# Optimization experiments

Hardware: AMD Instinct MI355X
Metric: run time of the kernel (lower is better)

Reference implementation:

```python
import jax, jax.numpy as jnp
import numpy as np

B, HQ, HKV, QL, SL = 2, 32, 8, 1024, 4096
HEAD_DIM, HALF, ROPE, RANK = 128, 64, 64, 512


def setup_inputs() -> dict:
    key = jax.random.key(0)
    ks = jax.random.split(key, 6)
    return {
        "Q": jax.random.normal(ks[0], (B, HQ, QL, HEAD_DIM), jnp.float32),
        "C_kv_t2": jax.random.normal(ks[1], (B, SL, RANK), jnp.float32),
        "K_rope_t2": jax.random.normal(ks[2], (B, HKV, SL, ROPE), jnp.float32),
        "U_l": jax.random.normal(ks[3], (HALF, HALF), jnp.float32) / 8.0,
        "W_UK": jax.random.normal(ks[4], (HEAD_DIM - ROPE, RANK), jnp.float32) / 8.0,
        "W_UV": jax.random.normal(ks[5], (RANK, HEAD_DIM), jnp.float32) / 8.0,
    }


def reference(Q, C_kv_t2, K_rope_t2, U_l, W_UK, W_UV):
    # --- absorb_and_score ---
    # Rotate each half of Q by U_l (applied as x @ U_l.T)
    Qx, Qy = Q[..., :HALF], Q[..., HALF:]
    Q_rot = jnp.concatenate([Qx @ U_l.T, Qy @ U_l.T], axis=-1)  # [B,HQ,QL,HEAD_DIM]
    Q_rope = Q_rot[..., :ROPE]                                   # [B,HQ,QL,ROPE]
    Q_nope = Q_rot[..., ROPE:]                                   # [B,HQ,QL,nope_dim]
    Q_abs = Q_nope @ W_UK                                        # [B,HQ,QL,RANK]
    scores_nope = jnp.einsum('bhqr,bsr->bhqs', Q_abs, C_kv_t2)   # [B,HQ,QL,SL]
    # GQA: group q-heads per kv-head instead of materializing repeat_interleave
    g = HQ // HKV
    Qr_g = Q_rope.reshape(B, HKV, g, QL, ROPE)
    scores_rope = jnp.einsum('bkgqr,bksr->bkgqs', Qr_g, K_rope_t2)
    scores = scores_nope + scores_rope.reshape(B, HQ, QL, SL)
    # --- softmax glue + decompress_value ---
    weights = jax.nn.softmax(scores, axis=-1)                    # [B,HQ,QL,SL]
    out_latent = jnp.einsum('bhqs,bsr->bhqr', weights, C_kv_t2)  # [B,HQ,QL,RANK]
    out = out_latent @ W_UV                                      # [B,HQ,QL,HEAD_DIM]
    return out
```

## Files before the change

### kernel.cpp

```cpp
#include <hip/hip_runtime.h>
#include <stdint.h>

#define B_N   2
#define HQ_N  32
#define HKV_N 8
#define QL_N  1024
#define SL_N  4096
#define DH_N  128
#define ROPE_N 64
#define RANK_N 512

typedef _Float16 f16;
typedef _Float16 half8 __attribute__((ext_vector_type(8)));
typedef __fp16 fp16x2 __attribute__((ext_vector_type(2)));
typedef float floatx16 __attribute__((ext_vector_type(16)));
typedef int int2v __attribute__((ext_vector_type(2)));

union H8 { half8 h; uint64_t q[2]; };
union PK2 { fp16x2 h; uint32_t u; };
union BFU { uint32_t u[4]; half8 h; };

__device__ inline half8 cvt8(float4 a, float4 b) {
  half8 o;
  o[0] = (f16)a.x; o[1] = (f16)a.y; o[2] = (f16)a.z; o[3] = (f16)a.w;
  o[4] = (f16)b.x; o[5] = (f16)b.y; o[6] = (f16)b.z; o[7] = (f16)b.w;
  return o;
}

__global__ __launch_bounds__(256) void k_convert(const float* __restrict__ Kr,
                                                 f16* __restrict__ Krf) {
  size_t idx = ((size_t)blockIdx.x * 256 + threadIdx.x) * 8;
  float4 a = *(const float4*)(Kr + idx);
  float4 b = *(const float4*)(Kr + idx + 4);
  *(half8*)(Krf + idx) = cvt8(a, b);
}

__global__ __launch_bounds__(256) void k_weights(const float* __restrict__ Ul,
                                                 const float* __restrict__ WUK,
                                                 const float* __restrict__ WUV,
                                                 f16* __restrict__ M2T2,
                                                 f16* __restrict__ WUKh,
                                                 f16* __restrict__ WUVT) {
  int idx = blockIdx.x * 256 + threadIdx.x;
  if (idx < 16384) {
    int c = idx >> 7, d = idx & 127;
    float v = 0.f;
    if (c < 64) { if (d >= 64) v = Ul[c * 64 + (d - 64)]; }
    else        { if (d < 64)  v = Ul[(c - 64) * 64 + d]; }
    M2T2[idx] = (f16)v;
  } else if (idx < 49152) {
    int i = idx - 16384;
    WUKh[i] = (f16)WUK[i];
  } else {
    int i = idx - 49152;
    int c = i >> 9, r = i & 511;
    WUVT[i] = (f16)WUV[r * 128 + c];
  }
}

__global__ __launch_bounds__(256) void k_kncw(const float* __restrict__ C,
                                              const f16* __restrict__ WUKh,
                                              const f16* __restrict__ WUVT,
                                              f16* __restrict__ Kn,
                                              f16* __restrict__ CWT) {
  int t = threadIdx.x;
  int wave = t >> 6, lane = t & 63, l31 = lane & 31, lhi = lane >> 5;
  int b = blockIdx.x >> 7, st = blockIdx.x & 127;
  int s0 = st * 32;
  const float* cp = C + ((size_t)b * SL_N + s0 + l31) * RANK_N + lhi * 8;
  floatx16 a0, a1;
#pragma unroll
  for (int r = 0; r < 16; r++) { a0[r] = 0.f; a1[r] = 0.f; }
#pragma unroll 4
  for (int kk = 0; kk < 32; ++kk) {
    float4 fa = *(const float4*)(cp + kk * 16);
    float4 fb = *(const float4*)(cp + kk * 16 + 4);
    half8 cf = cvt8(fa, fb);
    if (wave == 0) {
      half8 b0 = *(const half8*)(WUKh + (size_t)l31 * RANK_N + kk * 16 + lhi * 8);
      half8 b1 = *(const half8*)(WUKh + (size_t)(32 + l31) * RANK_N + kk * 16 + lhi * 8);
      a0 = __builtin_amdgcn_mfma_f32_32x32x16_f16(cf, b0, a0, 0, 0, 0);
      a1 = __builtin_amdgcn_mfma_f32_32x32x16_f16(cf, b1, a1, 0, 0, 0);
    } else if (wave == 1) {
      half8 w0 = *(const half8*)(WUVT + (size_t)l31 * RANK_N + kk * 16 + lhi * 8);
      a0 = __builtin_amdgcn_mfma_f32_32x32x16_f16(w0, cf, a0, 0, 0, 0);
    } else if (wave == 2) {
      half8 w1 = *(const half8*)(WUVT + (size_t)(32 + l31) * RANK_N + kk * 16 + lhi * 8);
      half8 w2 = *(const half8*)(WUVT + (size_t)(64 + l31) * RANK_N + kk * 16 + lhi * 8);
      a0 = __builtin_amdgcn_mfma_f32_32x32x16_f16(w1, cf, a0, 0, 0, 0);
      a1 = __builtin_amdgcn_mfma_f32_32x32x16_f16(w2, cf, a1, 0, 0, 0);
    } else {
      half8 w3 = *(const half8*)(WUVT + (size_t)(96 + l31) * RANK_N + kk * 16 + lhi * 8);
      a0 = __builtin_amdgcn_mfma_f32_32x32x16_f16(w3, cf, a0, 0, 0, 0);
    }
  }
  if (wave == 0) {
#pragma unroll
    for (int r = 0; r < 16; r++) {
      int row = (r & 3) + 8 * (r >> 2) + 4 * lhi;
      Kn[((size_t)b * SL_N + s0 + row) * 64 + l31]      = (f16)a0[r];
      Kn[((size_t)b * SL_N + s0 + row) * 64 + 32 + l31] = (f16)a1[r];
    }
  } else if (wave == 1) {
#pragma unroll
    for (int r = 0; r < 16; r++) {
      int row = (r & 3) + 8 * (r >> 2) + 4 * lhi;
      CWT[((size_t)b * DH_N + row) * SL_N + s0 + l31] = (f16)a0[r];
    }
  } else if (wave == 2) {
#pragma unroll
    for (int r = 0; r < 16; r++) {
      int row = (r & 3) + 8 * (r >> 2) + 4 * lhi;
      CWT[((size_t)b * DH_N + 32 + row) * SL_N + s0 + l31] = (f16)a0[r];
      CWT[((size_t)b * DH_N + 64 + row) * SL_N + s0 + l31] = (f16)a1[r];
    }
  } else {
#pragma unroll
    for (int r = 0; r < 16; r++) {
      int row = (r & 3) + 8 * (r >> 2) + 4 * lhi;
      CWT[((size_t)b * DH_N + 96 + row) * SL_N + s0 + l31] = (f16)a0[r];
    }
  }
}

#define KROW 132
#define CROW 68

__global__ __launch_bounds__(256, 2) void k_flash(
    const float* __restrict__ Q, const f16* __restrict__ M2T2,
    const f16* __restrict__ Kn, const f16* __restrict__ Krf,
    const f16* __restrict__ CWT, float* __restrict__ out) {
  __shared__ __align__(16) char smem[51712];
  f16* kbuf  = (f16*)smem;
  f16* cbuf0 = (f16*)(smem + 16896);
  f16* cbuf1 = (f16*)(smem + 34304);
  f16* qs    = (f16*)smem;
  float* ot  = (float*)smem;

  int t = threadIdx.x;
  int wave = t >> 6, lane = t & 63, l31 = lane & 31, lhi = lane >> 5;
  int qt = blockIdx.x & 7; int h = (blockIdx.x >> 3) & 31; int b = blockIdx.x >> 8;
  int kv = h >> 2;
  int qloc = wave * 32 + l31;

  const f16* Knb = Kn + (size_t)b * SL_N * 64;
  const f16* Kb  = Krf + (size_t)(b * HKV_N + kv) * SL_N * ROPE_N;
  const f16* Wb  = CWT + (size_t)b * DH_N * SL_N;

  int kr = t >> 3, kc = t & 7;
  int cA = t >> 2, cch = t & 3;
  const f16* pKn = Knb + (size_t)kr * 64 + kc * 8;
  const f16* pKr = Kb + (size_t)kr * ROPE_N + kc * 8;
  const f16* pW0 = Wb + (size_t)cA * SL_N;
  const f16* pW1 = Wb + (size_t)(64 + cA) * SL_N;
  int sw0 = ((cch) ^ (cA & 7)) * 8;
  int sw1 = ((cch + 4) ^ (cA & 7)) * 8;
  int rsw = l31 & 7;

  H8 a0, a1, r0, r1, c0, c1, c2, c3;
  a0.h = *(const half8*)(pKn);
  a1.h = *(const half8*)(pKn + 32 * 64);
  r0.h = *(const half8*)(pKr);
  r1.h = *(const half8*)(pKr + 32 * ROPE_N);
  c0.h = *(const half8*)(pW0 + cch * 8);
  c1.h = *(const half8*)(pW0 + (cch + 4) * 8);
  c2.h = *(const half8*)(pW1 + cch * 8);
  c3.h = *(const half8*)(pW1 + (cch + 4) * 8);

  {
    const float* qp = Q + ((size_t)(b * HQ_N + h) * QL_N + qt * 128 + wave * 32 + l31) * DH_N + lhi * 8;
    floatx16 acc[4];
#pragma unroll
    for (int ct = 0; ct < 4; ct++)
#pragma unroll
      for (int r = 0; r < 16; r++) acc[ct][r] = 0.f;
#pragma unroll
    for (int kk = 0; kk < 8; ++kk) {
      float4 fa = *(const float4*)(qp + kk * 16);
      float4 fb = *(const float4*)(qp + kk * 16 + 4);
      half8 af = cvt8(fa, fb);
#pragma unroll
      for (int ct = 0; ct < 4; ct++) {
        half8 bf = *(const half8*)(M2T2 + (size_t)(ct * 32 + l31) * 128 + kk * 16 + lhi * 8);
        acc[ct] = __builtin_amdgcn_mfma_f32_32x32x16_f16(af, bf, acc[ct], 0, 0, 0);
      }
    }
    const float LOG2E = 1.44269504f;
#pragma unroll
    for (int ct = 0; ct < 4; ct++)
#pragma unroll
      for (int r = 0; r < 16; r++) {
        int row = (r & 3) + 8 * (r >> 2) + 4 * lhi;
        qs[(wave * 32 + row) * 132 + ct * 32 + l31] = (f16)(acc[ct][r] * LOG2E);
      }
  }
  __syncthreads();
  half8 qf[8];
#pragma unroll
  for (int kk = 0; kk < 8; kk++)
    qf[kk] = *(const half8*)(qs + (size_t)qloc * 132 + kk * 16 + lhi * 8);
  __syncthreads();

  {
    uint64_t* d;
    d = (uint64_t*)(kbuf + kr * KROW + kc * 8);              d[0] = a0.q[0]; d[1] = a0.q[1];
    d = (uint64_t*)(kbuf + (kr + 32) * KROW + kc * 8);       d[0] = a1.q[0]; d[1] = a1.q[1];
    d = (uint64_t*)(kbuf + kr * KROW + 64 + kc * 8);         d[0] = r0.q[0]; d[1] = r0.q[1];
    d = (uint64_t*)(kbuf + (kr + 32) * KROW + 64 + kc * 8);  d[0] = r1.q[0]; d[1] = r1.q[1];
    d = (uint64_t*)(cbuf0 + cA * CROW + sw0);                d[0] = c0.q[0]; d[1] = c0.q[1];
    d = (uint64_t*)(cbuf0 + cA * CROW + sw1);                d[0] = c1.q[0]; d[1] = c1.q[1];
    d = (uint64_t*)(cbuf0 + (64 + cA) * CROW + sw0);         d[0] = c2.q[0]; d[1] = c2.q[1];
    d = (uint64_t*)(cbuf0 + (64 + cA) * CROW + sw1);         d[0] = c3.q[0]; d[1] = c3.q[1];
  }
  __syncthreads();

  floatx16 oacc[4];
#pragma unroll
  for (int ct = 0; ct < 4; ct++)
#pragma unroll
    for (int r = 0; r < 16; r++) oacc[ct][r] = 0.f;
  float m_run = -1e30f, l_run = 0.f;

  for (int it = 0; it < 64; ++it) {
    f16* cc = (it & 1) ? cbuf1 : cbuf0;
    f16* cn = (it & 1) ? cbuf0 : cbuf1;
    bool pre = it < 63;
    int s0n = (it + 1) * 64;
    if (pre) {
      size_t ko = (size_t)s0n * 64;
      a0.h = *(const half8*)(pKn + ko);
      a1.h = *(const half8*)(pKn + ko + 32 * 64);
      r0.h = *(const half8*)(pKr + ko);
      r1.h = *(const half8*)(pKr + ko + 32 * ROPE_N);
      c0.h = *(const half8*)(pW0 + s0n + cch * 8);
      c1.h = *(const half8*)(pW0 + s0n + (cch + 4) * 8);
      c2.h = *(const half8*)(pW1 + s0n + cch * 8);
      c3.h = *(const half8*)(pW1 + s0n + (cch + 4) * 8);
    }

    floatx16 sa0, sa1;
#pragma unroll
    for (int r = 0; r < 16; r++) { sa0[r] = 0.f; sa1[r] = 0.f; }
    const f16* ka0 = kbuf + l31 * KROW + lhi * 8;
    const f16* ka1 = kbuf + (32 + l31) * KROW + lhi * 8;
    __builtin_amdgcn_s_setprio(1);
#pragma unroll
    for (int kk = 0; kk < 8; kk++) {
      H8 x0, x1;
      const uint64_t* p0 = (const uint64_t*)(ka0 + kk * 16);
      const uint64_t* p1 = (const uint64_t*)(ka1 + kk * 16);
      x0.q[0] = p0[0]; x0.q[1] = p0[1];
      x1.q[0] = p1[0]; x1.q[1] = p1[1];
      sa0 = __builtin_amdgcn_mfma_f32_32x32x16_f16(x0.h, qf[kk], sa0, 0, 0, 0);
      sa1 = __builtin_amdgcn_mfma_f32_32x32x16_f16(x1.h, qf[kk], sa1, 0, 0, 0);
    }
    __builtin_amdgcn_s_setprio(0);
    __syncthreads();

    float mt = -1e30f;
#pragma unroll
    for (int r = 0; r < 16; r++) { mt = fmaxf(mt, sa0[r]); mt = fmaxf(mt, sa1[r]); }
    mt = fmaxf(mt, __shfl_xor(mt, 32, 64));
    if (__any(mt > m_run)) {
      float m_new = fmaxf(m_run, mt);
      float alpha = __builtin_amdgcn_exp2f(m_run - m_new);
      l_run *= alpha;
#pragma unroll
      for (int ct = 0; ct < 4; ct++)
#pragma unroll
        for (int r = 0; r < 16; r++) oacc[ct][r] *= alpha;
      m_run = m_new;
    }
    float psum = 0.f;
#pragma unroll
    for (int r = 0; r < 16; r++) { sa0[r] = __builtin_amdgcn_exp2f(sa0[r] - m_run); psum += sa0[r]; }
#pragma unroll
    for (int r = 0; r < 16; r++) { sa1[r] = __builtin_amdgcn_exp2f(sa1[r] - m_run); psum += sa1[r]; }
    psum += __shfl_xor(psum, 32, 64);
    l_run += psum;

    half8 bfr0, bfr1, bfr2, bfr3;
    {
      uint32_t pk[8];
#pragma unroll
      for (int g = 0; g < 8; ++g) {
        PK2 pu; pu.h = __builtin_amdgcn_cvt_pkrtz(sa0[2 * g], sa0[2 * g + 1]);
        pk[g] = pu.u;
      }
      int2v v0 = __builtin_amdgcn_permlane32_swap((int)pk[0], (int)pk[2], false, false);
      pk[0] = (uint32_t)v0.x; pk[2] = (uint32_t)v0.y;
      int2v v1 = __builtin_amdgcn_permlane32_swap((int)pk[1], (int)pk[3], false, false);
      pk[1] = (uint32_t)v1.x; pk[3] = (uint32_t)v1.y;
      int2v v2 = __builtin_amdgcn_permlane32_swap((int)pk[4], (int)pk[6], false, false);
      pk[4] = (uint32_t)v2.x; pk[6] = (uint32_t)v2.y;
      int2v v3 = __builtin_amdgcn_permlane32_swap((int)pk[5], (int)pk[7], false, false);
      pk[5] = (uint32_t)v3.x; pk[7] = (uint32_t)v3.y;
      BFU f0, f1;
      f0.u[0] = pk[0]; f0.u[1] = pk[1]; f0.u[2] = pk[2]; f0.u[3] = pk[3];
      f1.u[0] = pk[4]; f1.u[1] = pk[5]; f1.u[2] = pk[6]; f1.u[3] = pk[7];
      bfr0 = f0.h; bfr1 = f1.h;
    }
    {
      uint32_t pk[8];
#pragma unroll
      for (int g = 0; g < 8; ++g) {
        PK2 pu; pu.h = __builtin_amdgcn_cvt_pkrtz(sa1[2 * g], sa1[2 * g + 1]);
        pk[g] = pu.u;
      }
      int2v v0 = __builtin_amdgcn_permlane32_swap((int)pk[0], (int)pk[2], false, false);
      pk[0] = (uint32_t)v0.x; pk[2] = (uint32_t)v0.y;
      int2v v1 = __builtin_amdgcn_permlane32_swap((int)pk[1], (int)pk[3], false, false);
      pk[1] = (uint32_t)v1.x; pk[3] = (uint32_t)v1.y;
      int2v v2 = __builtin_amdgcn_permlane32_swap((int)pk[4], (int)pk[6], false, false);
      pk[4] = (uint32_t)v2.x; pk[6] = (uint32_t)v2.y;
      int2v v3 = __builtin_amdgcn_permlane32_swap((int)pk[5], (int)pk[7], false, false);
      pk[5] = (uint32_t)v3.x; pk[7] = (uint32_t)v3.y;
      BFU f0, f1;
      f0.u[0] = pk[0]; f0.u[1] = pk[1]; f0.u[2] = pk[2]; f0.u[3] = pk[3];
      f1.u[0] = pk[4]; f1.u[1] = pk[5]; f1.u[2] = pk[6]; f1.u[3] = pk[7];
      bfr2 = f0.h; bfr3 = f1.h;
    }

    __builtin_amdgcn_s_setprio(1);
#pragma unroll
    for (int ks = 0; ks < 4; ++ks) {
      half8 bfh = (ks == 0) ? bfr0 : (ks == 1) ? bfr1 : (ks == 2) ? bfr2 : bfr3;
#pragma unroll
      for (int ct = 0; ct < 4; ct++) {
        H8 af;
        const uint64_t* pa = (const uint64_t*)(cc + (ct * 32 + l31) * CROW +
                                               (((ks * 2 + lhi) ^ rsw) * 8));
        af.q[0] = pa[0]; af.q[1] = pa[1];
        oacc[ct] = __builtin_amdgcn_mfma_f32_32x32x16_f16(af.h, bfh, oacc[ct], 0, 0, 0);
      }
    }
    __builtin_amdgcn_s_setprio(0);

    if (pre) {
      uint64_t* d;
      d = (uint64_t*)(kbuf + kr * KROW + kc * 8);              d[0] = a0.q[0]; d[1] = a0.q[1];
      d = (uint64_t*)(kbuf + (kr + 32) * KROW + kc * 8);       d[0] = a1.q[0]; d[1] = a1.q[1];
      d = (uint64_t*)(kbuf + kr * KROW + 64 + kc * 8);         d[0] = r0.q[0]; d[1] = r0.q[1];
      d = (uint64_t*)(kbuf + (kr + 32) * KROW + 64 + kc * 8);  d[0] = r1.q[0]; d[1] = r1.q[1];
      d = (uint64_t*)(cn + cA * CROW + sw0);                   d[0] = c0.q[0]; d[1] = c0.q[1];
      d = (uint64_t*)(cn + cA * CROW + sw1);                   d[0] = c1.q[0]; d[1] = c1.q[1];
      d = (uint64_t*)(cn + (64 + cA) * CROW + sw0);            d[0] = c2.q[0]; d[1] = c2.q[1];
      d = (uint64_t*)(cn + (64 + cA) * CROW + sw1);            d[0] = c3.q[0]; d[1] = c3.q[1];
    }
    __syncthreads();
  }

  float inv = 1.0f / l_run;
  float* outp = out + ((size_t)(b * HQ_N + h) * QL_N + qt * 128) * DH_N;
#pragma unroll
  for (int p = 0; p < 2; ++p) {
    __syncthreads();
    if ((qloc >> 6) == p) {
      int lr = qloc & 63;
#pragma unroll
      for (int ct = 0; ct < 4; ct++)
#pragma unroll
        for (int r = 0; r < 16; r++) {
          int c = ct * 32 + (r & 3) + 8 * (r >> 2) + 4 * lhi;
          ot[lr * 133 + c] = oacc[ct][r] * inv;
        }
    }
    __syncthreads();
#pragma unroll
    for (int i = 0; i < 8; i++) {
      int flat = i * 256 + t; int q = flat >> 5, ch = flat & 31;
      float4 v;
      v.x = ot[q * 133 + ch * 4 + 0];
      v.y = ot[q * 133 + ch * 4 + 1];
      v.z = ot[q * 133 + ch * 4 + 2];
      v.w = ot[q * 133 + ch * 4 + 3];
      *(float4*)(outp + (size_t)(p * 64 + q) * DH_N + ch * 4) = v;
    }
  }
}

extern "C" void kernel_launch(void* const* d_in, const int* in_sizes, int n_in,
                              void* d_out, int out_size, void* d_ws, size_t ws_size,
                              hipStream_t stream) {
  (void)in_sizes; (void)n_in; (void)out_size; (void)ws_size;
  const float* Q   = (const float*)d_in[0];
  const float* C   = (const float*)d_in[1];
  const float* Kr  = (const float*)d_in[2];
  const float* Ul  = (const float*)d_in[3];
  const float* WUK = (const float*)d_in[4];
  const float* WUV = (const float*)d_in[5];
  float* out = (float*)d_out;
  char* ws = (char*)d_ws;
  f16* Krf   = (f16*)ws;
  f16* CWT   = (f16*)(ws + 8388608);
  f16* Kn    = (f16*)(ws + 10485760);
  f16* M2T2  = (f16*)(ws + 11534336);
  f16* WUKh  = (f16*)(ws + 11567104);
  f16* WUVT  = (f16*)(ws + 11632640);

  hipLaunchKernelGGL(k_convert, dim3(2048), dim3(256), 0, stream, Kr, Krf);
  hipLaunchKernelGGL(k_weights, dim3(448),  dim3(256), 0, stream, Ul, WUK, WUV, M2T2, WUKh, WUVT);
  hipLaunchKernelGGL(k_kncw,    dim3(256),  dim3(256), 0, stream, C, WUKh, WUVT, Kn, CWT);
  hipLaunchKernelGGL(k_flash,   dim3(512),  dim3(256), 0, stream, Q, M2T2, Kn, Krf, CWT, out);
}
```

Before: 287.7 us.

## Software-pipeline score MMA with softmax and PV in flash kernel

Restructures the flash loop so the QK^T MFMA for tile t+1 is issued while softmax and the PV MFMA run for tile t. The K tile is now double-buffered in LDS and global loads are prefetched two tiles ahead. This is meant to hide softmax latency and global-load latency behind matrix work, at the cost of more LDS (68.6 KB per block) and more register pressure. The C_kv fp32-to-fp16 conversion moves into the convert kernel, which adds a separate pass over C, and the max/sum reductions are split into independent chains for more ILP.

```diff
diff --git a/kernel.cpp b/kernel.cpp
--- a/kernel.cpp
+++ b/kernel.cpp
@@ -27,12 +27,19 @@
   return o;
 }
 
-__global__ __launch_bounds__(256) void k_convert(const float* __restrict__ Kr,
+__global__ __launch_bounds__(256) void k_convert(const float* __restrict__ C,
+                                                 const float* __restrict__ Kr,
+                                                 f16* __restrict__ Cf,
                                                  f16* __restrict__ Krf) {
+  const size_t NC = (size_t)B_N * SL_N * RANK_N;
   size_t idx = ((size_t)blockIdx.x * 256 + threadIdx.x) * 8;
-  float4 a = *(const float4*)(Kr + idx);
-  float4 b = *(const float4*)(Kr + idx + 4);
-  *(half8*)(Krf + idx) = cvt8(a, b);
+  const float* src;
+  f16* dst;
+  if (idx < NC) { src = C + idx;         dst = Cf + idx; }
+  else          { src = Kr + (idx - NC); dst = Krf + (idx - NC); }
+  float4 a = *(const float4*)(src);
+  float4 b = *(const float4*)(src + 4);
+  *(half8*)dst = cvt8(a, b);
 }
 
 __global__ __launch_bounds__(256) void k_weights(const float* __restrict__ Ul,
@@ -58,7 +65,7 @@
   }
 }
 
-__global__ __launch_bounds__(256) void k_kncw(const float* __restrict__ C,
+__global__ __launch_bounds__(256) void k_kncw(const f16* __restrict__ Cf,
                                               const f16* __restrict__ WUKh,
                                               const f16* __restrict__ WUVT,
                                               f16* __restrict__ Kn,
@@ -67,15 +74,13 @@
   int wave = t >> 6, lane = t & 63, l31 = lane & 31, lhi = lane >> 5;
   int b = blockIdx.x >> 7, st = blockIdx.x & 127;
   int s0 = st * 32;
-  const float* cp = C + ((size_t)b * SL_N + s0 + l31) * RANK_N + lhi * 8;
+  const f16* cp = Cf + ((size_t)b * SL_N + s0 + l31) * RANK_N + lhi * 8;
   floatx16 a0, a1;
 #pragma unroll
   for (int r = 0; r < 16; r++) { a0[r] = 0.f; a1[r] = 0.f; }
 #pragma unroll 4
   for (int kk = 0; kk < 32; ++kk) {
-    float4 fa = *(const float4*)(cp + kk * 16);
-    float4 fb = *(const float4*)(cp + kk * 16 + 4);
-    half8 cf = cvt8(fa, fb);
+    half8 cf = *(const half8*)(cp + kk * 16);
     if (wave == 0) {
       half8 b0 = *(const half8*)(WUKh + (size_t)l31 * RANK_N + kk * 16 + lhi * 8);
       half8 b1 = *(const half8*)(WUKh + (size_t)(32 + l31) * RANK_N + kk * 16 + lhi * 8);
@@ -130,10 +135,11 @@
     const float* __restrict__ Q, const f16* __restrict__ M2T2,
     const f16* __restrict__ Kn, const f16* __restrict__ Krf,
     const f16* __restrict__ CWT, float* __restrict__ out) {
-  __shared__ __align__(16) char smem[51712];
-  f16* kbuf  = (f16*)smem;
-  f16* cbuf0 = (f16*)(smem + 16896);
-  f16* cbuf1 = (f16*)(smem + 34304);
+  __shared__ __align__(16) char smem[68608];
+  f16* kbuf0 = (f16*)smem;
+  f16* kbuf1 = (f16*)(smem + 16896);
+  f16* cbuf0 = (f16*)(smem + 33792);
+  f16* cbuf1 = (f16*)(smem + 51200);
   f16* qs    = (f16*)smem;
   float* ot  = (float*)smem;
 
@@ -157,18 +163,36 @@
   int sw1 = ((cch + 4) ^ (cA & 7)) * 8;
   int rsw = l31 & 7;
 
-  H8 a0, a1, r0, r1, c0, c1, c2, c3;
-  a0.h = *(const half8*)(pKn);
-  a1.h = *(const half8*)(pKn + 32 * 64);
-  r0.h = *(const half8*)(pKr);
-  r1.h = *(const half8*)(pKr + 32 * ROPE_N);
-  c0.h = *(const half8*)(pW0 + cch * 8);
-  c1.h = *(const half8*)(pW0 + (cch + 4) * 8);
-  c2.h = *(const half8*)(pW1 + cch * 8);
-  c3.h = *(const half8*)(pW1 + (cch + 4) * 8);
-
+  H8 a0, a1, r0, r1, c0v, c1v, c2v, c3v;
+
+  auto issue = [&](int t2) {
+    size_t ko = (size_t)t2 * (64 * 64);
+    int soff = t2 * 64;
+    a0.h  = *(const half8*)(pKn + ko);
+    a1.h  = *(const half8*)(pKn + ko + 32 * 64);
+    r0.h  = *(const half8*)(pKr + ko);
+    r1.h  = *(const half8*)(pKr + ko + 32 * 64);
+    c0v.h = *(const half8*)(pW0 + soff + cch * 8);
+    c1v.h = *(const half8*)(pW0 + soff + (cch + 4) * 8);
+    c2v.h = *(const half8*)(pW1 + soff + cch * 8);
+    c3v.h = *(const half8*)(pW1 + soff + (cch + 4) * 8);
+  };
+  auto commit = [&](f16* kbW, f16* cbW) {
+    uint64_t* d;
+    d = (uint64_t*)(kbW + kr * KROW + kc * 8);             d[0] = a0.q[0]; d[1] = a0.q[1];
+    d = (uint64_t*)(kbW + (kr + 32) * KROW + kc * 8);      d[0] = a1.q[0]; d[1] = a1.q[1];
+    d = (uint64_t*)(kbW + kr * KROW + 64 + kc * 8);        d[0] = r0.q[0]; d[1] = r0.q[1];
+    d = (uint64_t*)(kbW + (kr + 32) * KROW + 64 + kc * 8); d[0] = r1.q[0]; d[1] = r1.q[1];
+    d = (uint64_t*)(cbW + cA * CROW + sw0);                d[0] = c0v.q[0]; d[1] = c0v.q[1];
+    d = (uint64_t*)(cbW + cA * CROW + sw1);                d[0] = c1v.q[0]; d[1] = c1v.q[1];
+    d = (uint64_t*)(cbW + (64 + cA) * CROW + sw0);         d[0] = c2v.q[0]; d[1] = c2v.q[1];
+    d = (uint64_t*)(cbW + (64 + cA) * CROW + sw1);         d[0] = c3v.q[0]; d[1] = c3v.q[1];
+  };
+
+  issue(0);
+  half8 qf[8];
   {
-    const float* qp = Q + ((size_t)(b * HQ_N + h) * QL_N + qt * 128 + wave * 32 + l31) * DH_N + lhi * 8;
+    const float* qp = Q + ((size_t)(b * HQ_N + h) * QL_N + qt * 128 + qloc) * DH_N + lhi * 8;
     floatx16 acc[4];
 #pragma unroll
     for (int ct = 0; ct < 4; ct++)
@@ -195,25 +219,11 @@
       }
   }
   __syncthreads();
-  half8 qf[8];
 #pragma unroll
   for (int kk = 0; kk < 8; kk++)
     qf[kk] = *(const half8*)(qs + (size_t)qloc * 132 + kk * 16 + lhi * 8);
   __syncthreads();
 
-  {
-    uint64_t* d;
-    d = (uint64_t*)(kbuf + kr * KROW + kc * 8);              d[0] = a0.q[0]; d[1] = a0.q[1];
-    d = (uint64_t*)(kbuf + (kr + 32) * KROW + kc * 8);       d[0] = a1.q[0]; d[1] = a1.q[1];
-    d = (uint64_t*)(kbuf + kr * KROW + 64 + kc * 8);         d[0] = r0.q[0]; d[1] = r0.q[1];
-    d = (uint64_t*)(kbuf + (kr + 32) * KROW + 64 + kc * 8);  d[0] = r1.q[0]; d[1] = r1.q[1];
-    d = (uint64_t*)(cbuf0 + cA * CROW + sw0);                d[0] = c0.q[0]; d[1] = c0.q[1];
-    d = (uint64_t*)(cbuf0 + cA * CROW + sw1);                d[0] = c1.q[0]; d[1] = c1.q[1];
-    d = (uint64_t*)(cbuf0 + (64 + cA) * CROW + sw0);         d[0] = c2.q[0]; d[1] = c2.q[1];
-    d = (uint64_t*)(cbuf0 + (64 + cA) * CROW + sw1);         d[0] = c3.q[0]; d[1] = c3.q[1];
-  }
-  __syncthreads();
-
   floatx16 oacc[4];
 #pragma unroll
   for (int ct = 0; ct < 4; ct++)
@@ -221,29 +231,11 @@
     for (int r = 0; r < 16; r++) oacc[ct][r] = 0.f;
   float m_run = -1e30f, l_run = 0.f;
 
-  for (int it = 0; it < 64; ++it) {
-    f16* cc = (it & 1) ? cbuf1 : cbuf0;
-    f16* cn = (it & 1) ? cbuf0 : cbuf1;
-    bool pre = it < 63;
-    int s0n = (it + 1) * 64;
-    if (pre) {
-      size_t ko = (size_t)s0n * 64;
-      a0.h = *(const half8*)(pKn + ko);
-      a1.h = *(const half8*)(pKn + ko + 32 * 64);
-      r0.h = *(const half8*)(pKr + ko);
-      r1.h = *(const half8*)(pKr + ko + 32 * ROPE_N);
-      c0.h = *(const half8*)(pW0 + s0n + cch * 8);
-      c1.h = *(const half8*)(pW0 + s0n + (cch + 4) * 8);
-      c2.h = *(const half8*)(pW1 + s0n + cch * 8);
-      c3.h = *(const half8*)(pW1 + s0n + (cch + 4) * 8);
-    }
-
-    floatx16 sa0, sa1;
-#pragma unroll
-    for (int r = 0; r < 16; r++) { sa0[r] = 0.f; sa1[r] = 0.f; }
-    const f16* ka0 = kbuf + l31 * KROW + lhi * 8;
-    const f16* ka1 = kbuf + (32 + l31) * KROW + lhi * 8;
-    __builtin_amdgcn_s_setprio(1);
+  auto stmm = [&](const f16* kbN, floatx16& n0, floatx16& n1) {
+#pragma unroll
+    for (int r = 0; r < 16; r++) { n0[r] = 0.f; n1[r] = 0.f; }
+    const f16* ka0 = kbN + l31 * KROW + lhi * 8;
+    const f16* ka1 = kbN + (32 + l31) * KROW + lhi * 8;
 #pragma unroll
     for (int kk = 0; kk < 8; kk++) {
       H8 x0, x1;
@@ -251,15 +243,20 @@
       const uint64_t* p1 = (const uint64_t*)(ka1 + kk * 16);
       x0.q[0] = p0[0]; x0.q[1] = p0[1];
       x1.q[0] = p1[0]; x1.q[1] = p1[1];
-      sa0 = __builtin_amdgcn_mfma_f32_32x32x16_f16(x0.h, qf[kk], sa0, 0, 0, 0);
-      sa1 = __builtin_amdgcn_mfma_f32_32x32x16_f16(x1.h, qf[kk], sa1, 0, 0, 0);
-    }
-    __builtin_amdgcn_s_setprio(0);
-    __syncthreads();
-
-    float mt = -1e30f;
-#pragma unroll
-    for (int r = 0; r < 16; r++) { mt = fmaxf(mt, sa0[r]); mt = fmaxf(mt, sa1[r]); }
+      n0 = __builtin_amdgcn_mfma_f32_32x32x16_f16(x0.h, qf[kk], n0, 0, 0, 0);
+      n1 = __builtin_amdgcn_mfma_f32_32x32x16_f16(x1.h, qf[kk], n1, 0, 0, 0);
+    }
+  };
+  auto softmax = [&](floatx16& s0, floatx16& s1) {
+    float u[8];
+#pragma unroll
+    for (int g = 0; g < 4; g++)
+      u[g] = fmaxf(fmaxf(s0[4 * g], s0[4 * g + 1]), fmaxf(s0[4 * g + 2], s0[4 * g + 3]));
+#pragma unroll
+    for (int g = 0; g < 4; g++)
+      u[4 + g] = fmaxf(fmaxf(s1[4 * g], s1[4 * g + 1]), fmaxf(s1[4 * g + 2], s1[4 * g + 3]));
+    float mt = fmaxf(fmaxf(fmaxf(u[0], u[1]), fmaxf(u[2], u[3])),
+                     fmaxf(fmaxf(u[4], u[5]), fmaxf(u[6], u[7])));
     mt = fmaxf(mt, __shfl_xor(mt, 32, 64));
     if (__any(mt > m_run)) {
       float m_new = fmaxf(m_run, mt);
@@ -271,83 +268,87 @@
         for (int r = 0; r < 16; r++) oacc[ct][r] *= alpha;
       m_run = m_new;
     }
-    float psum = 0.f;
-#pragma unroll
-    for (int r = 0; r < 16; r++) { sa0[r] = __builtin_amdgcn_exp2f(sa0[r] - m_run); psum += sa0[r]; }
-#pragma unroll
-    for (int r = 0; r < 16; r++) { sa1[r] = __builtin_amdgcn_exp2f(sa1[r] - m_run); psum += sa1[r]; }
+    float p0 = 0.f, p1 = 0.f, p2 = 0.f, p3 = 0.f;
+#pragma unroll
+    for (int r = 0; r < 16; r += 4) {
+      s0[r] = __builtin_amdgcn_exp2f(s0[r] - m_run);         p0 += s0[r];
+      s0[r + 1] = __builtin_amdgcn_exp2f(s0[r + 1] - m_run); p1 += s0[r + 1];
+      s0[r + 2] = __builtin_amdgcn_exp2f(s0[r + 2] - m_run); p2 += s0[r + 2];
+      s0[r + 3] = __builtin_amdgcn_exp2f(s0[r + 3] - m_run); p3 += s0[r + 3];
+    }
+#pragma unroll
+    for (int r = 0; r < 16; r += 4) {
+      s1[r] = __builtin_amdgcn_exp2f(s1[r] - m_run);         p0 += s1[r];
+      s1[r + 1] = __builtin_amdgcn_exp2f(s1[r + 1] - m_run); p1 += s1[r + 1];
+      s1[r + 2] = __builtin_amdgcn_exp2f(s1[r + 2] - m_run); p2 += s1[r + 2];
+      s1[r + 3] = __builtin_amdgcn_exp2f(s1[r + 3] - m_run); p3 += s1[r + 3];
+    }
+    float psum = (p0 + p1) + (p2 + p3);
     psum += __shfl_xor(psum, 32, 64);
     l_run += psum;
-
-    half8 bfr0, bfr1, bfr2, bfr3;
-    {
-      uint32_t pk[8];
-#pragma unroll
-      for (int g = 0; g < 8; ++g) {
-        PK2 pu; pu.h = __builtin_amdgcn_cvt_pkrtz(sa0[2 * g], sa0[2 * g + 1]);
-        pk[g] = pu.u;
-      }
-      int2v v0 = __builtin_amdgcn_permlane32_swap((int)pk[0], (int)pk[2], false, false);
-      pk[0] = (uint32_t)v0.x; pk[2] = (uint32_t)v0.y;
-      int2v v1 = __builtin_amdgcn_permlane32_swap((int)pk[1], (int)pk[3], false, false);
-      pk[1] = (uint32_t)v1.x; pk[3] = (uint32_t)v1.y;
-      int2v v2 = __builtin_amdgcn_permlane32_swap((int)pk[4], (int)pk[6], false, false);
-      pk[4] = (uint32_t)v2.x; pk[6] = (uint32_t)v2.y;
-      int2v v3 = __builtin_amdgcn_permlane32_swap((int)pk[5], (int)pk[7], false, false);
-      pk[5] = (uint32_t)v3.x; pk[7] = (uint32_t)v3.y;
-      BFU f0, f1;
-      f0.u[0] = pk[0]; f0.u[1] = pk[1]; f0.u[2] = pk[2]; f0.u[3] = pk[3];
-      f1.u[0] = pk[4]; f1.u[1] = pk[5]; f1.u[2] = pk[6]; f1.u[3] = pk[7];
-      bfr0 = f0.h; bfr1 = f1.h;
-    }
-    {
-      uint32_t pk[8];
-#pragma unroll
-      for (int g = 0; g < 8; ++g) {
-        PK2 pu; pu.h = __builtin_amdgcn_cvt_pkrtz(sa1[2 * g], sa1[2 * g + 1]);
-        pk[g] = pu.u;
-      }
-      int2v v0 = __builtin_amdgcn_permlane32_swap((int)pk[0], (int)pk[2], false, false);
-      pk[0] = (uint32_t)v0.x; pk[2] = (uint32_t)v0.y;
-      int2v v1 = __builtin_amdgcn_permlane32_swap((int)pk[1], (int)pk[3], false, false);
-      pk[1] = (uint32_t)v1.x; pk[3] = (uint32_t)v1.y;
-      int2v v2 = __builtin_amdgcn_permlane32_swap((int)pk[4], (int)pk[6], false, false);
-      pk[4] = (uint32_t)v2.x; pk[6] = (uint32_t)v2.y;
-      int2v v3 = __builtin_amdgcn_permlane32_swap((int)pk[5], (int)pk[7], false, false);
-      pk[5] = (uint32_t)v3.x; pk[7] = (uint32_t)v3.y;
-      BFU f0, f1;
-      f0.u[0] = pk[0]; f0.u[1] = pk[1]; f0.u[2] = pk[2]; f0.u[3] = pk[3];
-      f1.u[0] = pk[4]; f1.u[1] = pk[5]; f1.u[2] = pk[6]; f1.u[3] = pk[7];
-      bfr2 = f0.h; bfr3 = f1.h;
-    }
-
-    __builtin_amdgcn_s_setprio(1);
+  };
+  auto pack2 = [&](floatx16& s, half8& o0, half8& o1) {
+    uint32_t pk[8];
+#pragma unroll
+    for (int g = 0; g < 8; ++g) {
+      PK2 pu; pu.h = __builtin_amdgcn_cvt_pkrtz(s[2 * g], s[2 * g + 1]);
+      pk[g] = pu.u;
+    }
+    int2v v0 = __builtin_amdgcn_permlane32_swap((int)pk[0], (int)pk[2], false, false);
+    pk[0] = (uint32_t)v0.x; pk[2] = (uint32_t)v0.y;
+    int2v v1 = __builtin_amdgcn_permlane32_swap((int)pk[1], (int)pk[3], false, false);
+    pk[1] = (uint32_t)v1.x; pk[3] = (uint32_t)v1.y;
+    int2v v2 = __builtin_amdgcn_permlane32_swap((int)pk[4], (int)pk[6], false, false);
+    pk[4] = (uint32_t)v2.x; pk[6] = (uint32_t)v2.y;
+    int2v v3 = __builtin_amdgcn_permlane32_swap((int)pk[5], (int)pk[7], false, false);
+    pk[5] = (uint32_t)v3.x; pk[7] = (uint32_t)v3.y;
+    BFU f0, f1;
+    f0.u[0] = pk[0]; f0.u[1] = pk[1]; f0.u[2] = pk[2]; f0.u[3] = pk[3];
+    f1.u[0] = pk[4]; f1.u[1] = pk[5]; f1.u[2] = pk[6]; f1.u[3] = pk[7];
+    o0 = f0.h; o1 = f1.h;
+  };
+  auto pvmm = [&](const f16* cbC, half8 b0, half8 b1, half8 b2, half8 b3) {
 #pragma unroll
     for (int ks = 0; ks < 4; ++ks) {
-      half8 bfh = (ks == 0) ? bfr0 : (ks == 1) ? bfr1 : (ks == 2) ? bfr2 : bfr3;
+      half8 bfh = (ks == 0) ? b0 : (ks == 1) ? b1 : (ks == 2) ? b2 : b3;
 #pragma unroll
       for (int ct = 0; ct < 4; ct++) {
         H8 af;
-        const uint64_t* pa = (const uint64_t*)(cc + (ct * 32 + l31) * CROW +
+        const uint64_t* pa = (const uint64_t*)(cbC + (ct * 32 + l31) * CROW +
                                                (((ks * 2 + lhi) ^ rsw) * 8));
         af.q[0] = pa[0]; af.q[1] = pa[1];
         oacc[ct] = __builtin_amdgcn_mfma_f32_32x32x16_f16(af.h, bfh, oacc[ct], 0, 0, 0);
       }
     }
+  };
+
+  auto subit = [&](floatx16& cs0, floatx16& cs1, floatx16& ns0, floatx16& ns1,
+                   const f16* kbN, const f16* cbC, f16* kbW, f16* cbW, int tt) {
+    issue(tt + 2);
+    __builtin_amdgcn_s_setprio(1);
+    stmm(kbN, ns0, ns1);
+    softmax(cs0, cs1);
+    half8 b0, b1, b2, b3;
+    pack2(cs0, b0, b1);
+    pack2(cs1, b2, b3);
+    pvmm(cbC, b0, b1, b2, b3);
     __builtin_amdgcn_s_setprio(0);
-
-    if (pre) {
-      uint64_t* d;
-      d = (uint64_t*)(kbuf + kr * KROW + kc * 8);              d[0] = a0.q[0]; d[1] = a0.q[1];
-      d = (uint64_t*)(kbuf + (kr + 32) * KROW + kc * 8);       d[0] = a1.q[0]; d[1] = a1.q[1];
-      d = (uint64_t*)(kbuf + kr * KROW + 64 + kc * 8);         d[0] = r0.q[0]; d[1] = r0.q[1];
-      d = (uint64_t*)(kbuf + (kr + 32) * KROW + 64 + kc * 8);  d[0] = r1.q[0]; d[1] = r1.q[1];
-      d = (uint64_t*)(cn + cA * CROW + sw0);                   d[0] = c0.q[0]; d[1] = c0.q[1];
-      d = (uint64_t*)(cn + cA * CROW + sw1);                   d[0] = c1.q[0]; d[1] = c1.q[1];
-      d = (uint64_t*)(cn + (64 + cA) * CROW + sw0);            d[0] = c2.q[0]; d[1] = c2.q[1];
-      d = (uint64_t*)(cn + (64 + cA) * CROW + sw1);            d[0] = c3.q[0]; d[1] = c3.q[1];
-    }
     __syncthreads();
+    commit(kbW, cbW);
+    __syncthreads();
+  };
+
+  commit(kbuf0, cbuf0);
+  issue(1);
+  __syncthreads();
+  floatx16 saA0, saA1, saB0, saB1;
+  stmm(kbuf0, saA0, saA1);
+  commit(kbuf1, cbuf1);
+  __syncthreads();
+
+  for (int i2 = 0; i2 < 32; ++i2) {
+    subit(saA0, saA1, saB0, saB1, kbuf1, cbuf0, kbuf0, cbuf0, 2 * i2);
+    subit(saB0, saB1, saA0, saA1, kbuf0, cbuf1, kbuf1, cbuf1, 2 * i2 + 1);
   }
 
   float inv = 1.0f / l_run;
@@ -391,15 +392,16 @@
   const float* WUV = (const float*)d_in[5];
   float* out = (float*)d_out;
   char* ws = (char*)d_ws;
-  f16* Krf   = (f16*)ws;
-  f16* CWT   = (f16*)(ws + 8388608);
-  f16* Kn    = (f16*)(ws + 10485760);
-  f16* M2T2  = (f16*)(ws + 11534336);
-  f16* WUKh  = (f16*)(ws + 11567104);
-  f16* WUVT  = (f16*)(ws + 11632640);
-
-  hipLaunchKernelGGL(k_convert, dim3(2048), dim3(256), 0, stream, Kr, Krf);
+  f16* Cf    = (f16*)ws;
+  f16* Krf   = (f16*)(ws + 8388608);
+  f16* CWT   = (f16*)(ws + 16777216);
+  f16* Kn    = (f16*)(ws + 18874368);
+  f16* M2T2  = (f16*)(ws + 19922944);
+  f16* WUKh  = (f16*)(ws + 19955712);
+  f16* WUVT  = (f16*)(ws + 20021248);
+
+  hipLaunchKernelGGL(k_convert, dim3(4096), dim3(256), 0, stream, C, Kr, Cf, Krf);
   hipLaunchKernelGGL(k_weights, dim3(448),  dim3(256), 0, stream, Ul, WUK, WUV, M2T2, WUKh, WUVT);
-  hipLaunchKernelGGL(k_kncw,    dim3(256),  dim3(256), 0, stream, C, WUKh, WUVT, Kn, CWT);
+  hipLaunchKernelGGL(k_kncw,    dim3(256),  dim3(256), 0, stream, Cf, WUKh, WUVT, Kn, CWT);
   hipLaunchKernelGGL(k_flash,   dim3(512),  dim3(256), 0, stream, Q, M2T2, Kn, Krf, CWT, out);
 }
```

After: 286.3 us. Within noise of the previous version (-0.5%).

## Split KV sequence in two with merge kernel, single-buffer smem, lazy rescale

Applied to the files above, without the earlier changes.

The flash kernel now splits the 4096-long sequence into two halves. That doubles the grid to 1024 blocks, and each block writes unnormalized partial outputs plus running max and sum. A new merge kernel combines the two halves. Shared memory drops to one C buffer (two barriers per iteration), and launch bounds rise to allow four blocks per CU. The prep kernels are fused into one launch, and the online-softmax rescale is skipped unless the max grows by more than 12 in log2 units. This adds about 67 MB of fp32 partial-output traffic and an extra launch, and the lazy-rescale threshold allows exp2 values up to 2^12 before rescaling.

```diff
diff --git a/kernel.cpp b/kernel.cpp
--- a/kernel.cpp
+++ b/kernel.cpp
@@ -27,34 +27,36 @@
   return o;
 }
 
-__global__ __launch_bounds__(256) void k_convert(const float* __restrict__ Kr,
-                                                 f16* __restrict__ Krf) {
-  size_t idx = ((size_t)blockIdx.x * 256 + threadIdx.x) * 8;
-  float4 a = *(const float4*)(Kr + idx);
-  float4 b = *(const float4*)(Kr + idx + 4);
-  *(half8*)(Krf + idx) = cvt8(a, b);
-}
-
-__global__ __launch_bounds__(256) void k_weights(const float* __restrict__ Ul,
-                                                 const float* __restrict__ WUK,
-                                                 const float* __restrict__ WUV,
-                                                 f16* __restrict__ M2T2,
-                                                 f16* __restrict__ WUKh,
-                                                 f16* __restrict__ WUVT) {
-  int idx = blockIdx.x * 256 + threadIdx.x;
-  if (idx < 16384) {
-    int c = idx >> 7, d = idx & 127;
-    float v = 0.f;
-    if (c < 64) { if (d >= 64) v = Ul[c * 64 + (d - 64)]; }
-    else        { if (d < 64)  v = Ul[(c - 64) * 64 + d]; }
-    M2T2[idx] = (f16)v;
-  } else if (idx < 49152) {
-    int i = idx - 16384;
-    WUKh[i] = (f16)WUK[i];
+__global__ __launch_bounds__(256) void k_prep(const float* __restrict__ Kr,
+                                              const float* __restrict__ Ul,
+                                              const float* __restrict__ WUK,
+                                              const float* __restrict__ WUV,
+                                              f16* __restrict__ Krf,
+                                              f16* __restrict__ M2T2,
+                                              f16* __restrict__ WUKh,
+                                              f16* __restrict__ WUVT) {
+  int bid = blockIdx.x;
+  if (bid < 2048) {
+    size_t idx = ((size_t)bid * 256 + threadIdx.x) * 8;
+    float4 a = *(const float4*)(Kr + idx);
+    float4 b = *(const float4*)(Kr + idx + 4);
+    *(half8*)(Krf + idx) = cvt8(a, b);
   } else {
-    int i = idx - 49152;
-    int c = i >> 9, r = i & 511;
-    WUVT[i] = (f16)WUV[r * 128 + c];
+    int idx = (bid - 2048) * 256 + threadIdx.x;
+    if (idx < 16384) {
+      int c = idx >> 7, d = idx & 127;
+      float v = 0.f;
+      if (c < 64) { if (d >= 64) v = Ul[c * 64 + (d - 64)]; }
+      else        { if (d < 64)  v = Ul[(c - 64) * 64 + d]; }
+      M2T2[idx] = (f16)v;
+    } else if (idx < 49152) {
+      int i = idx - 16384;
+      WUKh[i] = (f16)WUK[i];
+    } else {
+      int i = idx - 49152;
+      int c = i >> 9, r = i & 511;
+      WUVT[i] = (f16)WUV[r * 128 + c];
+    }
   }
 }
 
@@ -126,22 +128,24 @@
 #define KROW 132
 #define CROW 68
 
-__global__ __launch_bounds__(256, 2) void k_flash(
+__global__ __launch_bounds__(256, 4) void k_flash(
     const float* __restrict__ Q, const f16* __restrict__ M2T2,
     const f16* __restrict__ Kn, const f16* __restrict__ Krf,
-    const f16* __restrict__ CWT, float* __restrict__ out) {
-  __shared__ __align__(16) char smem[51712];
-  f16* kbuf  = (f16*)smem;
-  f16* cbuf0 = (f16*)(smem + 16896);
-  f16* cbuf1 = (f16*)(smem + 34304);
-  f16* qs    = (f16*)smem;
-  float* ot  = (float*)smem;
+    const f16* __restrict__ CWT, float* __restrict__ Opart,
+    float* __restrict__ Ml) {
+  __shared__ __align__(16) char smem[34304];
+  f16* kbuf = (f16*)smem;
+  f16* cbuf = (f16*)(smem + 16896);
+  f16* qs   = (f16*)smem;
+  float* ot = (float*)smem;
 
   int t = threadIdx.x;
   int wave = t >> 6, lane = t & 63, l31 = lane & 31, lhi = lane >> 5;
-  int qt = blockIdx.x & 7; int h = (blockIdx.x >> 3) & 31; int b = blockIdx.x >> 8;
+  int rest = blockIdx.x & 511, half = blockIdx.x >> 9;
+  int qt = rest & 7; int h = (rest >> 3) & 31; int b = rest >> 8;
   int kv = h >> 2;
   int qloc = wave * 32 + l31;
+  int tb = half * 32;
 
   const f16* Knb = Kn + (size_t)b * SL_N * 64;
   const f16* Kb  = Krf + (size_t)(b * HKV_N + kv) * SL_N * ROPE_N;
@@ -149,26 +153,43 @@
 
   int kr = t >> 3, kc = t & 7;
   int cA = t >> 2, cch = t & 3;
-  const f16* pKn = Knb + (size_t)kr * 64 + kc * 8;
-  const f16* pKr = Kb + (size_t)kr * ROPE_N + kc * 8;
-  const f16* pW0 = Wb + (size_t)cA * SL_N;
-  const f16* pW1 = Wb + (size_t)(64 + cA) * SL_N;
+  const f16* pKn = Knb + (size_t)(tb * 64 + kr) * 64 + kc * 8;
+  const f16* pKr = Kb + (size_t)(tb * 64 + kr) * 64 + kc * 8;
+  const f16* pW0 = Wb + (size_t)cA * SL_N + tb * 64;
+  const f16* pW1 = Wb + (size_t)(64 + cA) * SL_N + tb * 64;
   int sw0 = ((cch) ^ (cA & 7)) * 8;
   int sw1 = ((cch + 4) ^ (cA & 7)) * 8;
   int rsw = l31 & 7;
 
-  H8 a0, a1, r0, r1, c0, c1, c2, c3;
-  a0.h = *(const half8*)(pKn);
-  a1.h = *(const half8*)(pKn + 32 * 64);
-  r0.h = *(const half8*)(pKr);
-  r1.h = *(const half8*)(pKr + 32 * ROPE_N);
-  c0.h = *(const half8*)(pW0 + cch * 8);
-  c1.h = *(const half8*)(pW0 + (cch + 4) * 8);
-  c2.h = *(const half8*)(pW1 + cch * 8);
-  c3.h = *(const half8*)(pW1 + (cch + 4) * 8);
-
+  H8 a0, a1, r0, r1, c0v, c1v, c2v, c3v;
+  auto issue = [&](int tt) {
+    size_t ko = (size_t)tt * (64 * 64);
+    int soff = tt * 64;
+    a0.h  = *(const half8*)(pKn + ko);
+    a1.h  = *(const half8*)(pKn + ko + 32 * 64);
+    r0.h  = *(const half8*)(pKr + ko);
+    r1.h  = *(const half8*)(pKr + ko + 32 * 64);
+    c0v.h = *(const half8*)(pW0 + soff + cch * 8);
+    c1v.h = *(const half8*)(pW0 + soff + (cch + 4) * 8);
+    c2v.h = *(const half8*)(pW1 + soff + cch * 8);
+    c3v.h = *(const half8*)(pW1 + soff + (cch + 4) * 8);
+  };
+  auto commit = [&]() {
+    uint64_t* d;
+    d = (uint64_t*)(kbuf + kr * KROW + kc * 8);             d[0] = a0.q[0]; d[1] = a0.q[1];
+    d = (uint64_t*)(kbuf + (kr + 32) * KROW + kc * 8);      d[0] = a1.q[0]; d[1] = a1.q[1];
+    d = (uint64_t*)(kbuf + kr * KROW + 64 + kc * 8);        d[0] = r0.q[0]; d[1] = r0.q[1];
+    d = (uint64_t*)(kbuf + (kr + 32) * KROW + 64 + kc * 8); d[0] = r1.q[0]; d[1] = r1.q[1];
+    d = (uint64_t*)(cbuf + cA * CROW + sw0);                d[0] = c0v.q[0]; d[1] = c0v.q[1];
+    d = (uint64_t*)(cbuf + cA * CROW + sw1);                d[0] = c1v.q[0]; d[1] = c1v.q[1];
+    d = (uint64_t*)(cbuf + (64 + cA) * CROW + sw0);         d[0] = c2v.q[0]; d[1] = c2v.q[1];
+    d = (uint64_t*)(cbuf + (64 + cA) * CROW + sw1);         d[0] = c3v.q[0]; d[1] = c3v.q[1];
+  };
+
+  issue(0);
+  half8 qf[8];
   {
-    const float* qp = Q + ((size_t)(b * HQ_N + h) * QL_N + qt * 128 + wave * 32 + l31) * DH_N + lhi * 8;
+    const float* qp = Q + ((size_t)(b * HQ_N + h) * QL_N + qt * 128 + qloc) * DH_N + lhi * 8;
     floatx16 acc[4];
 #pragma unroll
     for (int ct = 0; ct < 4; ct++)
@@ -195,23 +216,12 @@
       }
   }
   __syncthreads();
-  half8 qf[8];
 #pragma unroll
   for (int kk = 0; kk < 8; kk++)
     qf[kk] = *(const half8*)(qs + (size_t)qloc * 132 + kk * 16 + lhi * 8);
   __syncthreads();
-
-  {
-    uint64_t* d;
-    d = (uint64_t*)(kbuf + kr * KROW + kc * 8);              d[0] = a0.q[0]; d[1] = a0.q[1];
-    d = (uint64_t*)(kbuf + (kr + 32) * KROW + kc * 8);       d[0] = a1.q[0]; d[1] = a1.q[1];
-    d = (uint64_t*)(kbuf + kr * KROW + 64 + kc * 8);         d[0] = r0.q[0]; d[1] = r0.q[1];
-    d = (uint64_t*)(kbuf + (kr + 32) * KROW + 64 + kc * 8);  d[0] = r1.q[0]; d[1] = r1.q[1];
-    d = (uint64_t*)(cbuf0 + cA * CROW + sw0);                d[0] = c0.q[0]; d[1] = c0.q[1];
-    d = (uint64_t*)(cbuf0 + cA * CROW + sw1);                d[0] = c1.q[0]; d[1] = c1.q[1];
-    d = (uint64_t*)(cbuf0 + (64 + cA) * CROW + sw0);         d[0] = c2.q[0]; d[1] = c2.q[1];
-    d = (uint64_t*)(cbuf0 + (64 + cA) * CROW + sw1);         d[0] = c3.q[0]; d[1] = c3.q[1];
-  }
+  commit();
+  issue(1);
   __syncthreads();
 
   floatx16 oacc[4];
@@ -221,63 +231,67 @@
     for (int r = 0; r < 16; r++) oacc[ct][r] = 0.f;
   float m_run = -1e30f, l_run = 0.f;
 
-  for (int it = 0; it < 64; ++it) {
-    f16* cc = (it & 1) ? cbuf1 : cbuf0;
-    f16* cn = (it & 1) ? cbuf0 : cbuf1;
-    bool pre = it < 63;
-    int s0n = (it + 1) * 64;
-    if (pre) {
-      size_t ko = (size_t)s0n * 64;
-      a0.h = *(const half8*)(pKn + ko);
-      a1.h = *(const half8*)(pKn + ko + 32 * 64);
-      r0.h = *(const half8*)(pKr + ko);
-      r1.h = *(const half8*)(pKr + ko + 32 * ROPE_N);
-      c0.h = *(const half8*)(pW0 + s0n + cch * 8);
-      c1.h = *(const half8*)(pW0 + s0n + (cch + 4) * 8);
-      c2.h = *(const half8*)(pW1 + s0n + cch * 8);
-      c3.h = *(const half8*)(pW1 + s0n + (cch + 4) * 8);
-    }
-
+  for (int it = 0; it < 32; ++it) {
     floatx16 sa0, sa1;
 #pragma unroll
     for (int r = 0; r < 16; r++) { sa0[r] = 0.f; sa1[r] = 0.f; }
-    const f16* ka0 = kbuf + l31 * KROW + lhi * 8;
-    const f16* ka1 = kbuf + (32 + l31) * KROW + lhi * 8;
-    __builtin_amdgcn_s_setprio(1);
-#pragma unroll
-    for (int kk = 0; kk < 8; kk++) {
-      H8 x0, x1;
-      const uint64_t* p0 = (const uint64_t*)(ka0 + kk * 16);
-      const uint64_t* p1 = (const uint64_t*)(ka1 + kk * 16);
-      x0.q[0] = p0[0]; x0.q[1] = p0[1];
-      x1.q[0] = p1[0]; x1.q[1] = p1[1];
-      sa0 = __builtin_amdgcn_mfma_f32_32x32x16_f16(x0.h, qf[kk], sa0, 0, 0, 0);
-      sa1 = __builtin_amdgcn_mfma_f32_32x32x16_f16(x1.h, qf[kk], sa1, 0, 0, 0);
-    }
-    __builtin_amdgcn_s_setprio(0);
-    __syncthreads();
-
-    float mt = -1e30f;
-#pragma unroll
-    for (int r = 0; r < 16; r++) { mt = fmaxf(mt, sa0[r]); mt = fmaxf(mt, sa1[r]); }
-    mt = fmaxf(mt, __shfl_xor(mt, 32, 64));
-    if (__any(mt > m_run)) {
-      float m_new = fmaxf(m_run, mt);
-      float alpha = __builtin_amdgcn_exp2f(m_run - m_new);
-      l_run *= alpha;
-#pragma unroll
-      for (int ct = 0; ct < 4; ct++)
-#pragma unroll
-        for (int r = 0; r < 16; r++) oacc[ct][r] *= alpha;
-      m_run = m_new;
-    }
-    float psum = 0.f;
-#pragma unroll
-    for (int r = 0; r < 16; r++) { sa0[r] = __builtin_amdgcn_exp2f(sa0[r] - m_run); psum += sa0[r]; }
-#pragma unroll
-    for (int r = 0; r < 16; r++) { sa1[r] = __builtin_amdgcn_exp2f(sa1[r] - m_run); psum += sa1[r]; }
-    psum += __shfl_xor(psum, 32, 64);
-    l_run += psum;
+    {
+      const f16* ka0 = kbuf + l31 * KROW + lhi * 8;
+      const f16* ka1 = kbuf + (32 + l31) * KROW + lhi * 8;
+      __builtin_amdgcn_s_setprio(1);
+#pragma unroll
+      for (int kk = 0; kk < 8; kk++) {
+        H8 x0, x1;
+        const uint64_t* p0 = (const uint64_t*)(ka0 + kk * 16);
+        const uint64_t* p1 = (const uint64_t*)(ka1 + kk * 16);
+        x0.q[0] = p0[0]; x0.q[1] = p0[1];
+        x1.q[0] = p1[0]; x1.q[1] = p1[1];
+        sa0 = __builtin_amdgcn_mfma_f32_32x32x16_f16(x0.h, qf[kk], sa0, 0, 0, 0);
+        sa1 = __builtin_amdgcn_mfma_f32_32x32x16_f16(x1.h, qf[kk], sa1, 0, 0, 0);
+      }
+      __builtin_amdgcn_s_setprio(0);
+    }
+
+    {
+      float u0 = -1e30f, u1 = -1e30f, u2 = -1e30f, u3 = -1e30f;
+#pragma unroll
+      for (int r = 0; r < 16; r += 4) {
+        u0 = fmaxf(u0, fmaxf(sa0[r], sa1[r]));
+        u1 = fmaxf(u1, fmaxf(sa0[r + 1], sa1[r + 1]));
+        u2 = fmaxf(u2, fmaxf(sa0[r + 2], sa1[r + 2]));
+        u3 = fmaxf(u3, fmaxf(sa0[r + 3], sa1[r + 3]));
+      }
+      float mt = fmaxf(fmaxf(u0, u1), fmaxf(u2, u3));
+      mt = fmaxf(mt, __shfl_xor(mt, 32, 64));
+      if (__any(mt > m_run + 12.f)) {
+        float m_new = fmaxf(m_run, mt);
+        float alpha = __builtin_amdgcn_exp2f(m_run - m_new);
+        l_run *= alpha;
+#pragma unroll
+        for (int ct = 0; ct < 4; ct++)
+#pragma unroll
+          for (int r = 0; r < 16; r++) oacc[ct][r] *= alpha;
+        m_run = m_new;
+      }
+      float p0 = 0.f, p1 = 0.f, p2 = 0.f, p3 = 0.f;
+#pragma unroll
+      for (int r = 0; r < 16; r += 4) {
+        sa0[r] = __builtin_amdgcn_exp2f(sa0[r] - m_run);         p0 += sa0[r];
+        sa0[r + 1] = __builtin_amdgcn_exp2f(sa0[r + 1] - m_run); p1 += sa0[r + 1];
+        sa0[r + 2] = __builtin_amdgcn_exp2f(sa0[r + 2] - m_run); p2 += sa0[r + 2];
+        sa0[r + 3] = __builtin_amdgcn_exp2f(sa0[r + 3] - m_run); p3 += sa0[r + 3];
+      }
+#pragma unroll
+      for (int r = 0; r < 16; r += 4) {
+        sa1[r] = __builtin_amdgcn_exp2f(sa1[r] - m_run);         p0 += sa1[r];
+        sa1[r + 1] = __builtin_amdgcn_exp2f(sa1[r + 1] - m_run); p1 += sa1[r + 1];
+        sa1[r + 2] = __builtin_amdgcn_exp2f(sa1[r + 2] - m_run); p2 += sa1[r + 2];
+        sa1[r + 3] = __builtin_amdgcn_exp2f(sa1[r + 3] - m_run); p3 += sa1[r + 3];
+      }
+      float psum = (p0 + p1) + (p2 + p3);
+      psum += __shfl_xor(psum, 32, 64);
+      l_run += psum;
+    }
 
     half8 bfr0, bfr1, bfr2, bfr3;
     {
@@ -328,7 +342,7 @@
 #pragma unroll
       for (int ct = 0; ct < 4; ct++) {
         H8 af;
-        const uint64_t* pa = (const uint64_t*)(cc + (ct * 32 + l31) * CROW +
+        const uint64_t* pa = (const uint64_t*)(cbuf + (ct * 32 + l31) * CROW +
                                                (((ks * 2 + lhi) ^ rsw) * 8));
         af.q[0] = pa[0]; af.q[1] = pa[1];
         oacc[ct] = __builtin_amdgcn_mfma_f32_32x32x16_f16(af.h, bfh, oacc[ct], 0, 0, 0);
@@ -336,22 +350,13 @@
     }
     __builtin_amdgcn_s_setprio(0);
 
-    if (pre) {
-      uint64_t* d;
-      d = (uint64_t*)(kbuf + kr * KROW + kc * 8);              d[0] = a0.q[0]; d[1] = a0.q[1];
-      d = (uint64_t*)(kbuf + (kr + 32) * KROW + kc * 8);       d[0] = a1.q[0]; d[1] = a1.q[1];
-      d = (uint64_t*)(kbuf + kr * KROW + 64 + kc * 8);         d[0] = r0.q[0]; d[1] = r0.q[1];
-      d = (uint64_t*)(kbuf + (kr + 32) * KROW + 64 + kc * 8);  d[0] = r1.q[0]; d[1] = r1.q[1];
-      d = (uint64_t*)(cn + cA * CROW + sw0);                   d[0] = c0.q[0]; d[1] = c0.q[1];
-      d = (uint64_t*)(cn + cA * CROW + sw1);                   d[0] = c1.q[0]; d[1] = c1.q[1];
-      d = (uint64_t*)(cn + (64 + cA) * CROW + sw0);            d[0] = c2.q[0]; d[1] = c2.q[1];
-      d = (uint64_t*)(cn + (64 + cA) * CROW + sw1);            d[0] = c3.q[0]; d[1] = c3.q[1];
-    }
     __syncthreads();
-  }
-
-  float inv = 1.0f / l_run;
-  float* outp = out + ((size_t)(b * HQ_N + h) * QL_N + qt * 128) * DH_N;
+    commit();
+    issue(it + 2);
+    __syncthreads();
+  }
+
+  float* opb = Opart + (size_t)blockIdx.x * (128 * 128);
 #pragma unroll
   for (int p = 0; p < 2; ++p) {
     __syncthreads();
@@ -362,7 +367,7 @@
 #pragma unroll
         for (int r = 0; r < 16; r++) {
           int c = ct * 32 + (r & 3) + 8 * (r >> 2) + 4 * lhi;
-          ot[lr * 133 + c] = oacc[ct][r] * inv;
+          ot[lr * 133 + c] = oacc[ct][r];
         }
     }
     __syncthreads();
@@ -374,8 +379,47 @@
       v.y = ot[q * 133 + ch * 4 + 1];
       v.z = ot[q * 133 + ch * 4 + 2];
       v.w = ot[q * 133 + ch * 4 + 3];
-      *(float4*)(outp + (size_t)(p * 64 + q) * DH_N + ch * 4) = v;
-    }
+      *(float4*)(opb + (size_t)(p * 64 + q) * 128 + ch * 4) = v;
+    }
+  }
+  if (lane < 32) {
+    float* mlb = Ml + (size_t)blockIdx.x * 256;
+    mlb[qloc * 2]     = m_run;
+    mlb[qloc * 2 + 1] = l_run;
+  }
+}
+
+__global__ __launch_bounds__(256) void k_merge(const float* __restrict__ Opart,
+                                               const float* __restrict__ Ml,
+                                               float* __restrict__ out) {
+  __shared__ float sm[512];
+  int rest = blockIdx.x;
+  int t = threadIdx.x;
+  sm[t] = Ml[(size_t)rest * 256 + t];
+  sm[256 + t] = Ml[(size_t)(512 + rest) * 256 + t];
+  __syncthreads();
+  int qt = rest & 7; int h = (rest >> 3) & 31; int b = rest >> 8;
+  const float* O0 = Opart + (size_t)rest * 16384;
+  const float* O1 = Opart + (size_t)(512 + rest) * 16384;
+  float* dst = out + ((size_t)(b * HQ_N + h) * QL_N + qt * 128) * DH_N;
+#pragma unroll
+  for (int i = 0; i < 16; i++) {
+    int flat = i * 1024 + t * 4;
+    int q = flat >> 7;
+    float m0 = sm[q * 2], l0 = sm[q * 2 + 1];
+    float m1 = sm[256 + q * 2], l1 = sm[256 + q * 2 + 1];
+    float m = fmaxf(m0, m1);
+    float a0 = exp2f(m0 - m), a1 = exp2f(m1 - m);
+    float inv = 1.f / (l0 * a0 + l1 * a1);
+    a0 *= inv; a1 *= inv;
+    float4 v0 = *(const float4*)(O0 + flat);
+    float4 v1 = *(const float4*)(O1 + flat);
+    float4 o;
+    o.x = v0.x * a0 + v1.x * a1;
+    o.y = v0.y * a0 + v1.y * a1;
+    o.z = v0.z * a0 + v1.z * a1;
+    o.w = v0.w * a0 + v1.w * a1;
+    *(float4*)(dst + flat) = o;
   }
 }
 
@@ -391,15 +435,17 @@
   const float* WUV = (const float*)d_in[5];
   float* out = (float*)d_out;
   char* ws = (char*)d_ws;
-  f16* Krf   = (f16*)ws;
-  f16* CWT   = (f16*)(ws + 8388608);
-  f16* Kn    = (f16*)(ws + 10485760);
-  f16* M2T2  = (f16*)(ws + 11534336);
-  f16* WUKh  = (f16*)(ws + 11567104);
-  f16* WUVT  = (f16*)(ws + 11632640);
-
-  hipLaunchKernelGGL(k_convert, dim3(2048), dim3(256), 0, stream, Kr, Krf);
-  hipLaunchKernelGGL(k_weights, dim3(448),  dim3(256), 0, stream, Ul, WUK, WUV, M2T2, WUKh, WUVT);
-  hipLaunchKernelGGL(k_kncw,    dim3(256),  dim3(256), 0, stream, C, WUKh, WUVT, Kn, CWT);
-  hipLaunchKernelGGL(k_flash,   dim3(512),  dim3(256), 0, stream, Q, M2T2, Kn, Krf, CWT, out);
-}
+  f16* Krf    = (f16*)ws;
+  f16* CWT    = (f16*)(ws + 8388608);
+  f16* Kn     = (f16*)(ws + 10485760);
+  f16* M2T2   = (f16*)(ws + 11534336);
+  f16* WUKh   = (f16*)(ws + 11567104);
+  f16* WUVT   = (f16*)(ws + 11632640);
+  float* Opart= (float*)(ws + 11763712);
+  float* Ml   = (float*)(ws + 78872576);
+
+  hipLaunchKernelGGL(k_prep,  dim3(2496), dim3(256), 0, stream, Kr, Ul, WUK, WUV, Krf, M2T2, WUKh, WUVT);
+  hipLaunchKernelGGL(k_kncw,  dim3(256),  dim3(256), 0, stream, C, WUKh, WUVT, Kn, CWT);
+  hipLaunchKernelGGL(k_flash, dim3(1024), dim3(256), 0, stream, Q, M2T2, Kn, Krf, CWT, Opart, Ml);
+  hipLaunchKernelGGL(k_merge, dim3(512),  dim3(256), 0, stream, Opart, Ml, out);
+}
```

Result: slower. 619.1 us (+115.2%).
